# Kernel optimization log

Measured on AMD Instinct MI355X. Metric: run time of the kernel, lower is better.

## Reference

```python
import jax, jax.numpy as jnp
import numpy as np

B, WK, HRS = 2048, 52, 8760
DT = 0.125          # Euler step in days (3-hourly), exactly representable
RANGE_PRED = 7      # forecast horizon in days


def setup_inputs() -> dict:
    key = jax.random.key(0)
    k1, k2, k3, k4 = jax.random.split(key, 4)
    # X_in: [B, weeks, 5, 1]; channel 0 = start time in days (same across batch,
    # the torch code reads X_in[0, week, 0, 0]); channels 1..4 = N,P,Z,D init.
    X_in = jax.random.uniform(k1, (B, WK, 5, 1), jnp.float32, 0.1, 3.0)
    t0 = jnp.arange(WK, dtype=jnp.float32) * 7.0
    X_in = X_in.at[:, :, 0, 0].set(jnp.broadcast_to(t0, (B, WK)))
    global_f = jax.random.uniform(k2, (B, HRS), jnp.float32)          # light forcing in [0,1]
    global_m = jax.random.uniform(k3, (B, HRS), jnp.float32) * 0.1    # mixing rate, small
    params_value = jax.random.uniform(k4, (B, 10), jnp.float32, 0.1, 1.0)
    return {"X_in": X_in, "global_f": global_f, "global_m": global_m,
            "params_value": params_value, "dt": DT, "range_pred": RANGE_PRED}


def reference(X_in, global_f, global_m, params_value, dt, range_pred):
    # Fixed multipliers from the torch code
    pv = jnp.asarray([1.0, 2.0, 0.1, 0.05, 0.1, 0.3, 0.6, 0.15, 0.4, 0.1], X_in.dtype)
    Q0, Vm, thr = 8.0, 1.0, 0.01  # Q0 = 4 + 2.5 + 1.5 + 0
    chi, rho, gam, lam, eps, alp, bet, eta, phi, zet = [params_value[:, i][:, None] for i in range(10)]  # [B,1]

    n_steps = int(round(range_pred / dt))      # 56
    stride = int(round(1.0 / dt))              # 8 -> daily sampling of output

    # Hourly forcing gather: same time axis for every batch element (torch uses X_in[0,...])
    t0 = X_in[0, :, 0, 0]                                                     # [W]
    times = t0[:, None] + jnp.arange(n_steps + 1, dtype=X_in.dtype) * dt      # [W, S]
    idx = jnp.round(times * 24.0).astype(jnp.int32)
    f = jnp.take(global_f, idx, axis=1)[:, :, :n_steps]                       # [B, W, T]
    m = jnp.take(global_m, idx, axis=1)[:, :, :n_steps]

    def step(carry, ft_mt):
        N, P, Z, D = carry                      # each [B, W]
        ft, mt = ft_mt
        Pc = jnp.maximum(thr, P)
        Zc = jnp.maximum(thr, Z)
        gN = N / (chi * pv[0] + N)
        zg = rho * pv[1] * (1.0 - jnp.exp(-lam * pv[3] * Pc)) * Zc
        up = Vm * gN * ft * Pc
        Nn = N + dt * (-up + alp * pv[5] * zg + eps * pv[4] * P + gam * pv[2] * Z + phi * pv[8] * D + mt * (Q0 - N))
        Pn = P + dt * (up - zg - eps * pv[4] * P - eta * pv[7] * P - mt * P)
        Zn = Z + dt * (bet * pv[6] * zg - gam * pv[2] * Z - mt * Z)
        Dn = D + dt * (eta * pv[7] * P + (1.0 - alp * pv[5] - bet * pv[6]) * zg - phi * pv[8] * D - zet * pv[9] * D - mt * D)
        new = (Nn, Pn, Zn, Dn)
        return new, jnp.stack(new, axis=0)      # [4, B, W]

    carry0 = (X_in[:, :, 1, 0], X_in[:, :, 2, 0], X_in[:, :, 3, 0], X_in[:, :, 4, 0])
    _, ys = jax.lax.scan(step, carry0, (jnp.moveaxis(f, 2, 0), jnp.moveaxis(m, 2, 0)))  # ys: [T, 4, B, W]
    traj = jnp.concatenate([jnp.stack(carry0, axis=0)[None], ys], axis=0)               # [S, 4, B, W]
    out = jnp.moveaxis(traj, (0, 1), (3, 2))                                            # [B, W, 4, S]
    return out[:, :, :, ::stride]               # daily samples: [B, W, 4, range_pred+1]
```

## Files before the change

### kernel.cpp

```cpp
#include <hip/hip_runtime.h>


typedef float f32x4 __attribute__((ext_vector_type(4)));

#define NPZD_B 2048
#define NPZD_WK 52
#define NPZD_HRS 8760

__global__ __launch_bounds__(64, 2) void npzd_kernel(
    const float* __restrict__ X_in,
    const float* __restrict__ gf,
    const float* __restrict__ gm,
    const float* __restrict__ params,
    const float* __restrict__ dt_ptr,
    float* __restrict__ out)
{
    const int b    = blockIdx.x;
    const int lane = threadIdx.x;
    const int w    = (lane < NPZD_WK) ? lane : (NPZD_WK - 1);

    const f32x4* __restrict__ gfw = (const f32x4*)(gf + (size_t)b * NPZD_HRS) + 42 * w;
    const f32x4* __restrict__ gmw = (const f32x4*)(gm + (size_t)b * NPZD_HRS) + 42 * w;

    f32x4 fA0 = gfw[0], fA1 = gfw[1], fA2 = gfw[2];
    f32x4 mA0 = gmw[0], mA1 = gmw[1], mA2 = gmw[2];
    f32x4 fB0, fB1, fB2, mB0, mB1, mB2;

    const float dt = dt_ptr[0];
    const float* xb = X_in + ((size_t)b * NPZD_WK + w) * 5;
    float N = xb[1], P = xb[2], Z = xb[3], D = xb[4];

    const float* pp = params + (size_t)b * 10;
    const float chi   = pp[0];
    const float rho2  = pp[1] * 2.0f;
    const float gam1  = pp[2] * 0.1f;
    const float lam05 = pp[3] * 0.05f;
    const float eps1  = pp[4] * 0.1f;
    const float alp3  = pp[5] * 0.3f;
    const float bet6  = pp[6] * 0.6f;
    const float eta15 = pp[7] * 0.15f;
    const float phi4  = pp[8] * 0.4f;
    const float zet1  = pp[9] * 0.1f;
    const float rem   = 1.0f - alp3 - bet6;

    float oN[8], oP[8], oZ[8], oD[8];
    oN[0] = N; oP[0] = P; oZ[0] = Z; oD[0] = D;

    #pragma unroll
    for (int g = 0; g < 14; ++g) {
        const bool even = (g & 1) == 0;

        if (g < 13) {
            const f32x4* pf = gfw + 3 * (g + 1);
            const f32x4* pm = gmw + 3 * (g + 1);
            if (even) {
                fB0 = pf[0]; fB1 = pf[1]; fB2 = pf[2];
                mB0 = pm[0]; mB1 = pm[1]; mB2 = pm[2];
            } else {
                fA0 = pf[0]; fA1 = pf[1]; fA2 = pf[2];
                mA0 = pm[0]; mA1 = pm[1]; mA2 = pm[2];
            }
        }

        const f32x4 cf0 = even ? fA0 : fB0;
        const f32x4 cf1 = even ? fA1 : fB1;
        const f32x4 cf2 = even ? fA2 : fB2;
        const f32x4 cm0 = even ? mA0 : mB0;
        const f32x4 cm1 = even ? mA1 : mB1;
        const f32x4 cm2 = even ? mA2 : mB2;
        const float fs[4] = {cf0.x, cf0.w, cf1.z, cf2.y};
        const float ms[4] = {cm0.x, cm0.w, cm1.z, cm2.y};

        #pragma unroll
        for (int q = 0; q < 4; ++q) {
            const float ft = fs[q], mt = ms[q];
            const float Pc = fmaxf(0.01f, P);
            const float Zc = fmaxf(0.01f, Z);
            const float gN = N * __builtin_amdgcn_rcpf(chi + N);
            const float zg = rho2 * (1.0f - __expf(-lam05 * Pc)) * Zc;
            const float up = gN * ft * Pc;
            const float Nn = N + dt * (-up + alp3 * zg + eps1 * P + gam1 * Z + phi4 * D + mt * (8.0f - N));
            const float Pn = P + dt * (up - zg - eps1 * P - eta15 * P - mt * P);
            const float Zn = Z + dt * (bet6 * zg - gam1 * Z - mt * Z);
            const float Dn = D + dt * (eta15 * P + rem * zg - phi4 * D - zet1 * D - mt * D);
            N = Nn; P = Pn; Z = Zn; D = Dn;
        }
        if (g & 1) {
            const int c = (g >> 1) + 1;
            oN[c] = N; oP[c] = P; oZ[c] = Z; oD[c] = D;
        }
    }

    if (lane >= NPZD_WK) return;
    f32x4* o4 = (f32x4*)(out + ((size_t)b * NPZD_WK + w) * 32);
    o4[0] = (f32x4){oN[0], oN[1], oN[2], oN[3]};
    o4[1] = (f32x4){oN[4], oN[5], oN[6], oN[7]};
    o4[2] = (f32x4){oP[0], oP[1], oP[2], oP[3]};
    o4[3] = (f32x4){oP[4], oP[5], oP[6], oP[7]};
    o4[4] = (f32x4){oZ[0], oZ[1], oZ[2], oZ[3]};
    o4[5] = (f32x4){oZ[4], oZ[5], oZ[6], oZ[7]};
    o4[6] = (f32x4){oD[0], oD[1], oD[2], oD[3]};
    o4[7] = (f32x4){oD[4], oD[5], oD[6], oD[7]};
}

extern "C" void kernel_launch(void* const* d_in, const int* in_sizes, int n_in,
                              void* d_out, int out_size, void* d_ws, size_t ws_size,
                              hipStream_t stream) {
    const float* X_in   = (const float*)d_in[0];
    const float* gf     = (const float*)d_in[1];
    const float* gm     = (const float*)d_in[2];
    const float* params = (const float*)d_in[3];
    const float* dt_ptr = (const float*)d_in[4];
    float* out = (float*)d_out;

    npzd_kernel<<<NPZD_B, 64, 0, stream>>>(X_in, gf, gm, params, dt_ptr, out);
}
```

Baseline: 208.2 us.

## Split each batch into four blocks and stage forcing via direct global-to-LDS loads

```diff
diff --git a/kernel.cpp b/kernel.cpp
--- a/kernel.cpp
+++ b/kernel.cpp
@@ -6,8 +6,15 @@
 #define NPZD_B 2048
 #define NPZD_WK 52
 #define NPZD_HRS 8760
+#define NPZD_QW 13
+#define NPZD_QF4 546
+#define NPZD_PF4 576
+#define NPZD_MAXF4 2189
 
-__global__ __launch_bounds__(64, 2) void npzd_kernel(
+typedef const __attribute__((address_space(1))) void* gas_t;
+typedef __attribute__((address_space(3))) void* las_t;
+
+__global__ __launch_bounds__(64) void npzd_kernel(
     const float* __restrict__ X_in,
     const float* __restrict__ gf,
     const float* __restrict__ gm,
@@ -15,19 +22,32 @@
     const float* __restrict__ dt_ptr,
     float* __restrict__ out)
 {
-    const int b    = blockIdx.x;
+    __shared__ __align__(16) f32x4 lf4[NPZD_PF4];
+    __shared__ __align__(16) f32x4 lm4[NPZD_PF4];
+
+    const int bid  = blockIdx.x;
+    const int b    = bid >> 2;
+    const int qb   = bid & 3;
     const int lane = threadIdx.x;
-    const int w    = (lane < NPZD_WK) ? lane : (NPZD_WK - 1);
 
-    const f32x4* __restrict__ gfw = (const f32x4*)(gf + (size_t)b * NPZD_HRS) + 42 * w;
-    const f32x4* __restrict__ gmw = (const f32x4*)(gm + (size_t)b * NPZD_HRS) + 42 * w;
+    const f32x4* __restrict__ gf4 = (const f32x4*)(gf + (size_t)b * NPZD_HRS);
+    const f32x4* __restrict__ gm4 = (const f32x4*)(gm + (size_t)b * NPZD_HRS);
 
-    f32x4 fA0 = gfw[0], fA1 = gfw[1], fA2 = gfw[2];
-    f32x4 mA0 = gmw[0], mA1 = gmw[1], mA2 = gmw[2];
-    f32x4 fB0, fB1, fB2, mB0, mB1, mB2;
+    const int base = NPZD_QF4 * qb;
+    #pragma unroll
+    for (int i = 0; i < 9; ++i) {
+        int idx = base + i * 64 + lane;
+        if (idx > NPZD_MAXF4) idx = NPZD_MAXF4;
+        __builtin_amdgcn_global_load_lds((gas_t)(const void*)(gf4 + idx),
+                                         (las_t)(void*)&lf4[i * 64], 16, 0, 0);
+        __builtin_amdgcn_global_load_lds((gas_t)(const void*)(gm4 + idx),
+                                         (las_t)(void*)&lm4[i * 64], 16, 0, 0);
+    }
 
     const float dt = dt_ptr[0];
-    const float* xb = X_in + ((size_t)b * NPZD_WK + w) * 5;
+    const int wl = (lane < NPZD_QW) ? lane : (NPZD_QW - 1);
+    const int wg = NPZD_QW * qb + wl;
+    const float* xb = X_in + ((size_t)b * NPZD_WK + wg) * 5;
     float N = xb[1], P = xb[2], Z = xb[3], D = xb[4];
 
     const float* pp = params + (size_t)b * 10;
@@ -43,37 +63,23 @@
     const float zet1  = pp[9] * 0.1f;
     const float rem   = 1.0f - alp3 - bet6;
 
+    __syncthreads();
+
+    if (lane >= NPZD_QW) return;
+
     float oN[8], oP[8], oZ[8], oD[8];
     oN[0] = N; oP[0] = P; oZ[0] = Z; oD[0] = D;
 
+    const float* lf = (const float*)lf4 + 168 * wl;
+    const float* lm = (const float*)lm4 + 168 * wl;
+
     #pragma unroll
     for (int g = 0; g < 14; ++g) {
-        const bool even = (g & 1) == 0;
-
-        if (g < 13) {
-            const f32x4* pf = gfw + 3 * (g + 1);
-            const f32x4* pm = gmw + 3 * (g + 1);
-            if (even) {
-                fB0 = pf[0]; fB1 = pf[1]; fB2 = pf[2];
-                mB0 = pm[0]; mB1 = pm[1]; mB2 = pm[2];
-            } else {
-                fA0 = pf[0]; fA1 = pf[1]; fA2 = pf[2];
-                mA0 = pm[0]; mA1 = pm[1]; mA2 = pm[2];
-            }
-        }
-
-        const f32x4 cf0 = even ? fA0 : fB0;
-        const f32x4 cf1 = even ? fA1 : fB1;
-        const f32x4 cf2 = even ? fA2 : fB2;
-        const f32x4 cm0 = even ? mA0 : mB0;
-        const f32x4 cm1 = even ? mA1 : mB1;
-        const f32x4 cm2 = even ? mA2 : mB2;
-        const float fs[4] = {cf0.x, cf0.w, cf1.z, cf2.y};
-        const float ms[4] = {cm0.x, cm0.w, cm1.z, cm2.y};
-
         #pragma unroll
         for (int q = 0; q < 4; ++q) {
-            const float ft = fs[q], mt = ms[q];
+            const int s = 4 * g + q;
+            const float ft = lf[3 * s];
+            const float mt = lm[3 * s];
             const float Pc = fmaxf(0.01f, P);
             const float Zc = fmaxf(0.01f, Z);
             const float gN = N * __builtin_amdgcn_rcpf(chi + N);
@@ -91,8 +97,7 @@
         }
     }
 
-    if (lane >= NPZD_WK) return;
-    f32x4* o4 = (f32x4*)(out + ((size_t)b * NPZD_WK + w) * 32);
+    f32x4* o4 = (f32x4*)(out + ((size_t)b * NPZD_WK + wg) * 32);
     o4[0] = (f32x4){oN[0], oN[1], oN[2], oN[3]};
     o4[1] = (f32x4){oN[4], oN[5], oN[6], oN[7]};
     o4[2] = (f32x4){oP[0], oP[1], oP[2], oP[3]};
@@ -113,5 +118,5 @@
     const float* dt_ptr = (const float*)d_in[4];
     float* out = (float*)d_out;
 
-    npzd_kernel<<<NPZD_B, 64, 0, stream>>>(X_in, gf, gm, params, dt_ptr, out);
+    npzd_kernel<<<NPZD_B * 4, 64, 0, stream>>>(X_in, gf, gm, params, dt_ptr, out);
 }
```

Measured after the change: 183.1 us. 1.14x faster.
